# Kernel tuning notes

Measured on AMD Instinct MI355X. Metric: run time of the kernel, lower is better.

Reference implementation:

```python
import jax, jax.numpy as jnp
import numpy as np

VTH = 1.0  # config['v_threshold']
DT = 1.0


def spike_fn(x):
    # forward of ActFun_adp: heaviside(mem - vth)
    return (x > 0).astype(x.dtype)


def setup_inputs() -> dict:
    key = jax.random.key(0)
    k0, k1, k2, k3, k4 = jax.random.split(key, 5)
    B, T, D, H, O = 256, 250, 700, 1024, 20
    input_data = jax.random.normal(k0, (B, T, D), dtype=jnp.float32)
    # dense_1: nn.Linear(700, hidden) default init ~ U(-1/sqrt(D), 1/sqrt(D)); normal/sqrt(D) is an equivalent-scale stand-in
    W1 = jax.random.normal(k1, (H, D), dtype=jnp.float32) / np.sqrt(D).astype(np.float32)
    b1 = jnp.zeros((H,), dtype=jnp.float32)
    tau_m1 = jax.random.uniform(k2, (H,), dtype=jnp.float32, minval=0.0, maxval=4.0)
    # dense_2: xavier_normal_ weight, zero bias
    W2 = jax.random.normal(k3, (O, H), dtype=jnp.float32) * np.sqrt(2.0 / (H + O)).astype(np.float32)
    b2 = jnp.zeros((O,), dtype=jnp.float32)
    tau_m2 = jax.random.uniform(k4, (O,), dtype=jnp.float32, minval=0.0, maxval=4.0)
    return {"input_data": input_data, "W1": W1, "b1": b1, "tau_m1": tau_m1,
            "W2": W2, "b2": b2, "tau_m2": tau_m2}


def reference(input_data, W1, b1, tau_m1, W2, b2, tau_m2):
    B, T, D = input_data.shape
    H = W1.shape[0]
    O = W2.shape[0]
    alpha1 = jax.nn.sigmoid(tau_m1)  # [H]
    alpha2 = jax.nn.sigmoid(tau_m2)  # [O]
    # dense_1 is time-invariant: precompute projections for all timesteps [T,B,H]
    d1_all = (jnp.einsum('btd,hd->bth', input_data, W1) + b1).transpose(1, 0, 2)

    def step(carry, xs):
        mem1, spk1, mem2, acc = carry
        d1_t, i = xs
        # LIF layer 1: soft reset via -vth*spike (mem_update_pra, R_m=1, dt=1)
        mem1 = mem1 * alpha1 + (1.0 - alpha1) * d1_t - VTH * spk1 * DT
        spk1 = spike_fn(mem1 - VTH)
        # readout integrator
        d2 = spk1 @ W2.T + b2
        mem2 = mem2 * alpha2 + (1.0 - alpha2) * d2
        # accumulate softmax for i > 10
        gate = jnp.where(i > 10, jnp.float32(1.0), jnp.float32(0.0))
        acc = acc + gate * jax.nn.softmax(mem2, axis=1)
        return (mem1, spk1, mem2, acc), None

    init = (jnp.zeros((B, H), jnp.float32), jnp.zeros((B, H), jnp.float32),
            jnp.zeros((B, O), jnp.float32), jnp.zeros((B, O), jnp.float32))
    (_, _, _, acc), _ = jax.lax.scan(step, init, (d1_all, jnp.arange(T)))
    return acc
```

## Files before the change

kernel.cpp:

```cpp
#include <hip/hip_runtime.h>
#include <hip/hip_bf16.h>

#define B_  256
#define T_  250
#define D_  700
#define H_  1024
#define O_  20
#define KP  704
#define M_  64000

typedef __attribute__((ext_vector_type(8))) short bf16x8;
typedef __attribute__((ext_vector_type(4))) float f32x4;

__device__ __forceinline__ void gl_lds16(const void* g, void* l) {
    __builtin_amdgcn_global_load_lds(
        (const __attribute__((address_space(1))) unsigned int*)g,
        (__attribute__((address_space(3))) unsigned int*)l, 16, 0, 0);
}

__global__ void split_convert(const float* __restrict__ src,
                              unsigned short* __restrict__ hi,
                              unsigned short* __restrict__ lo,
                              int M, int Kin, int Kout)
{
    int idx = blockIdx.x * blockDim.x + threadIdx.x;
    int chunks = Kout >> 3;
    int total = M * chunks;
    if (idx >= total) return;
    int m  = idx / chunks;
    int c  = idx - m * chunks;
    int d0 = c << 3;
    float x[8];
    if (d0 + 8 <= Kin) {
        const float4* p = (const float4*)(src + (long)m * Kin + d0);
        float4 v0 = p[0], v1 = p[1];
        x[0] = v0.x; x[1] = v0.y; x[2] = v0.z; x[3] = v0.w;
        x[4] = v1.x; x[5] = v1.y; x[6] = v1.z; x[7] = v1.w;
    } else {
#pragma unroll
        for (int e = 0; e < 8; ++e) {
            int d = d0 + e;
            x[e] = (d < Kin) ? src[(long)m * Kin + d] : 0.0f;
        }
    }
    unsigned short h8[8], l8[8];
#pragma unroll
    for (int e = 0; e < 8; ++e) {
        __hip_bfloat16 h = __float2bfloat16(x[e]);
        float hf = __bfloat162float(h);
        __hip_bfloat16 lv = __float2bfloat16(x[e] - hf);
        h8[e] = *(unsigned short*)&h;
        l8[e] = *(unsigned short*)&lv;
    }
    long ob = (long)m * Kout + d0;
    *(uint4*)(hi + ob) = *(uint4*)h8;
    *(uint4*)(lo + ob) = *(uint4*)l8;
}

__global__ __launch_bounds__(256, 4) void gemm_split(
    const unsigned short* __restrict__ Ahi, const unsigned short* __restrict__ Alo,
    const unsigned short* __restrict__ Bhi, const unsigned short* __restrict__ Blo,
    const float* __restrict__ bias, float* __restrict__ C)
{
    __shared__ __align__(16) unsigned short sAh[128 * 32];
    __shared__ __align__(16) unsigned short sAl[128 * 32];
    __shared__ __align__(16) unsigned short sBh[128 * 32];
    __shared__ __align__(16) unsigned short sBl[128 * 32];

    const int t    = threadIdx.x;
    const int nblk = blockIdx.x;
    const int mblk = blockIdx.y;
    const int wave = t >> 6, lane = t & 63;
    const int wr = wave >> 1, wc = wave & 1;

    f32x4 acc[4][4];
#pragma unroll
    for (int i = 0; i < 4; ++i)
#pragma unroll
        for (int j = 0; j < 4; ++j) acc[i][j] = (f32x4){0.f, 0.f, 0.f, 0.f};

    const long arow = (long)(mblk * 128 + (t >> 2)) * KP + (t & 3) * 8;
    const long brow = (long)(nblk * 128 + (t >> 2)) * KP + (t & 3) * 8;
    const int  l8   = t * 8;

    const int fr = lane & 15;
    const int fk = (lane >> 4) * 8;

    for (int ks = 0; ks < KP; ks += 32) {
        __syncthreads();
        gl_lds16(Ahi + arow + ks, &sAh[l8]);
        gl_lds16(Ahi + arow + 64 * KP + ks, &sAh[2048 + l8]);
        gl_lds16(Alo + arow + ks, &sAl[l8]);
        gl_lds16(Alo + arow + 64 * KP + ks, &sAl[2048 + l8]);
        gl_lds16(Bhi + brow + ks, &sBh[l8]);
        gl_lds16(Bhi + brow + 64 * KP + ks, &sBh[2048 + l8]);
        gl_lds16(Blo + brow + ks, &sBl[l8]);
        gl_lds16(Blo + brow + 64 * KP + ks, &sBl[2048 + l8]);
        __syncthreads();

        bf16x8 bh[4], bl[4];
#pragma unroll
        for (int j = 0; j < 4; ++j) {
            bh[j] = *(const bf16x8*)&sBh[(wc * 64 + j * 16 + fr) * 32 + fk];
            bl[j] = *(const bf16x8*)&sBl[(wc * 64 + j * 16 + fr) * 32 + fk];
        }
#pragma unroll
        for (int i = 0; i < 4; ++i) {
            bf16x8 ah = *(const bf16x8*)&sAh[(wr * 64 + i * 16 + fr) * 32 + fk];
            bf16x8 al = *(const bf16x8*)&sAl[(wr * 64 + i * 16 + fr) * 32 + fk];
#pragma unroll
            for (int j = 0; j < 4; ++j)
                acc[i][j] = __builtin_amdgcn_mfma_f32_16x16x32_bf16(ah, bh[j], acc[i][j], 0, 0, 0);
#pragma unroll
            for (int j = 0; j < 4; ++j)
                acc[i][j] = __builtin_amdgcn_mfma_f32_16x16x32_bf16(ah, bl[j], acc[i][j], 0, 0, 0);
#pragma unroll
            for (int j = 0; j < 4; ++j)
                acc[i][j] = __builtin_amdgcn_mfma_f32_16x16x32_bf16(al, bh[j], acc[i][j], 0, 0, 0);
        }
    }

    const int r0 = mblk * 128 + wr * 64 + (lane >> 4) * 4;
    const int c0 = nblk * 128 + wc * 64 + (lane & 15);
#pragma unroll
    for (int j = 0; j < 4; ++j) {
        int col = c0 + j * 16;
        float bv = bias[col];
#pragma unroll
        for (int i = 0; i < 4; ++i) {
            int row = r0 + i * 16;
#pragma unroll
            for (int r = 0; r < 4; ++r)
                C[(long)(row + r) * H_ + col] = acc[i][j][r] + bv;
        }
    }
}

__global__ __launch_bounds__(256) void lif_spikes(
    const float* __restrict__ d1,
    const float* __restrict__ tau1,
    unsigned long long* __restrict__ spk)
{
    const int b    = blockIdx.y;
    const int h    = blockIdx.x * 256 + threadIdx.x;
    const int lane = threadIdx.x & 63;
    const int widx = blockIdx.x * 4 + (threadIdx.x >> 6);

    float tv  = tau1[h];
    float a1  = 1.0f / (1.0f + __expf(-tv));
    float om1 = 1.0f - a1;
    float mem = 0.f, sp = 0.f;

    const float* dp = d1 + (long)b * T_ * H_ + h;
    unsigned long long* op = spk + (long)b * T_ * 16 + widx;

    float p0 = dp[0],        p1 = dp[1L * H_], p2 = dp[2L * H_];
    float p3 = dp[3L * H_],  p4 = dp[4L * H_], p5 = dp[5L * H_];

    for (int ts = 0; ts < T_; ++ts) {
        float cur = p0;
        p0 = p1; p1 = p2; p2 = p3; p3 = p4; p4 = p5;
        int nts = ts + 6; nts = (nts < T_) ? nts : (T_ - 1);
        p5 = dp[(long)nts * H_];

        mem = mem * a1 + om1 * cur - sp;
        sp  = (mem > 1.0f) ? 1.0f : 0.0f;
        unsigned long long msk = __ballot(mem > 1.0f);
        if (lane == 0) op[(long)ts * 16] = msk;
    }
}

__global__ __launch_bounds__(256) void readout_dots(
    const unsigned long long* __restrict__ spk,
    const float* __restrict__ W2,
    float* __restrict__ d2t)
{
    const int t = threadIdx.x, wave = t >> 6, lane = t & 63;

    float w2r[5][16];
#pragma unroll
    for (int oo = 0; oo < 5; ++oo)
#pragma unroll
        for (int q = 0; q < 4; ++q)
            *(float4*)&w2r[oo][4 * q] =
                *(const float4*)&W2[(wave * 5 + oo) * H_ + lane * 16 + 4 * q];

    const int rbase = blockIdx.x * 32;
    int b0 = rbase / T_;
    int ts0 = rbase - b0 * T_;

    for (int i = 0; i < 32; i += 2) {
        int r0 = rbase + i, r1 = r0 + 1;
        unsigned long long bw0 = spk[(long)r0 * 16 + (lane >> 2)];
        unsigned long long bw1 = spk[(long)r1 * 16 + (lane >> 2)];
        unsigned int bits0 = (unsigned int)(bw0 >> ((lane & 3) * 16)) & 0xFFFFu;
        unsigned int bits1 = (unsigned int)(bw1 >> ((lane & 3) * 16)) & 0xFFFFu;
        float pa0[5] = {0, 0, 0, 0, 0}, pa1[5] = {0, 0, 0, 0, 0};
#pragma unroll
        for (int j = 0; j < 16; ++j) {
            float f0 = (bits0 >> j) & 1u ? 1.0f : 0.0f;
            float f1 = (bits1 >> j) & 1u ? 1.0f : 0.0f;
#pragma unroll
            for (int oo = 0; oo < 5; ++oo) {
                pa0[oo] = fmaf(f0, w2r[oo][j], pa0[oo]);
                pa1[oo] = fmaf(f1, w2r[oo][j], pa1[oo]);
            }
        }
#pragma unroll
        for (int m = 1; m < 64; m <<= 1)
#pragma unroll
            for (int oo = 0; oo < 5; ++oo) {
                pa0[oo] += __shfl_xor(pa0[oo], m, 64);
                pa1[oo] += __shfl_xor(pa1[oo], m, 64);
            }
        if (lane == 0) {
            int bA = b0, tsA = ts0 + i;
            if (tsA >= T_) { tsA -= T_; bA += 1; }
            int bB = bA, tsB = tsA + 1;
            if (tsB >= T_) { tsB = 0; bB += 1; }
#pragma unroll
            for (int oo = 0; oo < 5; ++oo) {
                d2t[(long)(wave * 5 + oo) * M_ + tsA * 256 + bA] = pa0[oo];
                d2t[(long)(wave * 5 + oo) * M_ + tsB * 256 + bB] = pa1[oo];
            }
        }
    }
}

__global__ __launch_bounds__(64) void mem2_scan(
    const float* __restrict__ d2t,
    const float* __restrict__ tau2, const float* __restrict__ b2,
    float* __restrict__ m2t)
{
    const int o = blockIdx.x;
    const int b = blockIdx.y * 64 + threadIdx.x;
    float tv  = tau2[o];
    float a2  = 1.0f / (1.0f + __expf(-tv));
    float om2 = 1.0f - a2;
    float bv  = b2[o];

    const float* dp = d2t + (long)o * M_ + b;
    float*       mp = m2t + (long)o * M_ + b;
    float mem = 0.f;

    float p0 = dp[0], p1 = dp[256], p2 = dp[512], p3 = dp[768];
    for (int ts = 0; ts < T_; ++ts) {
        float cur = p0; p0 = p1; p1 = p2; p2 = p3;
        int nts = ts + 4; nts = (nts < T_) ? nts : (T_ - 1);
        p3 = dp[(long)nts * 256];
        mem = mem * a2 + om2 * (cur + bv);
        mp[(long)ts * 256] = mem;
    }
}

__global__ __launch_bounds__(256) void softmax_acc(
    const float* __restrict__ m2t,
    float* __restrict__ out)
{
    __shared__ float sp[T_][O_];
    const int b  = blockIdx.x;
    const int ts = threadIdx.x;

    if (ts < T_) {
        if (ts > 10) {
            float m[O_];
#pragma unroll
            for (int o = 0; o < O_; ++o)
                m[o] = m2t[(long)o * M_ + ts * 256 + b];
            float mx = m[0];
#pragma unroll
            for (int o = 1; o < O_; ++o) mx = fmaxf(mx, m[o]);
            float s = 0.f;
#pragma unroll
            for (int o = 0; o < O_; ++o) { m[o] = __expf(m[o] - mx); s += m[o]; }
            float inv = 1.0f / s;
#pragma unroll
            for (int o = 0; o < O_; ++o) sp[ts][o] = m[o] * inv;
        } else {
#pragma unroll
            for (int o = 0; o < O_; ++o) sp[ts][o] = 0.f;
        }
    }
    __syncthreads();
    if (ts < O_) {
        float s = 0.f;
        for (int k = 11; k < T_; ++k) s += sp[k][ts];
        out[b * O_ + ts] = s;
    }
}

extern "C" void kernel_launch(void* const* d_in, const int* in_sizes, int n_in,
                              void* d_out, int out_size, void* d_ws, size_t ws_size,
                              hipStream_t stream)
{
    const float* X    = (const float*)d_in[0];
    const float* W1   = (const float*)d_in[1];
    const float* b1   = (const float*)d_in[2];
    const float* tau1 = (const float*)d_in[3];
    const float* W2   = (const float*)d_in[4];
    const float* b2   = (const float*)d_in[5];
    const float* tau2 = (const float*)d_in[6];
    float* out = (float*)d_out;

    unsigned short* Xhi  = (unsigned short*)d_ws;
    unsigned short* Xlo  = Xhi + (long)M_ * KP;
    unsigned short* W1hi = Xlo + (long)M_ * KP;
    unsigned short* W1lo = W1hi + (long)H_ * KP;
    float* d1 = (float*)(W1lo + (long)H_ * KP);

    unsigned long long* spk = (unsigned long long*)Xhi;
    float* d2t = (float*)Xlo;
    float* m2t = d2t + (long)O_ * M_;

    {
        int chunks = M_ * (KP / 8);
        split_convert<<<(chunks + 255) / 256, 256, 0, stream>>>(X, Xhi, Xlo, M_, D_, KP);
    }
    {
        int chunks = H_ * (KP / 8);
        split_convert<<<(chunks + 255) / 256, 256, 0, stream>>>(W1, W1hi, W1lo, H_, D_, KP);
    }

    {
        dim3 grid(H_ / 128, M_ / 128);
        gemm_split<<<grid, 256, 0, stream>>>(Xhi, Xlo, W1hi, W1lo, b1, d1);
    }

    {
        dim3 grid(H_ / 256, B_);
        lif_spikes<<<grid, 256, 0, stream>>>(d1, tau1, spk);
    }

    readout_dots<<<M_ / 32, 256, 0, stream>>>(spk, W2, d2t);

    {
        dim3 grid(O_, 4);
        mem2_scan<<<grid, 64, 0, stream>>>(d2t, tau2, b2, m2t);
    }

    softmax_acc<<<B_, 256, 0, stream>>>(m2t, out);
}
```

Before: 795.7 us.

## Replace split-bf16 GEMM with 256x256 double-buffered, swizzled, XCD-remapped kernel

Swaps the 128x128 split-bf16 GEMM for a 256x256 tile kernel with 512 threads, double-buffered LDS, and prefetch of the next K slice while the current one runs on MFMA. The LDS layout is XOR-swizzled to avoid bank conflicts, block IDs are remapped across the 8 XCDs for L2 locality, and s_setprio raises priority during MFMA bursts. The aim is more operand reuse per tile and overlap of global loads with compute. The cost is much higher register and LDS pressure (128 KB LDS, 32 accumulators per thread), and the hand-placed waitcnt and barrier scheduling is fragile.

```diff
diff --git a/kernel.cpp b/kernel.cpp
--- a/kernel.cpp
+++ b/kernel.cpp
@@ -8,6 +8,7 @@
 #define O_  20
 #define KP  704
 #define M_  64000
+#define NT  22
 
 typedef __attribute__((ext_vector_type(8))) short bf16x8;
 typedef __attribute__((ext_vector_type(4))) float f32x4;
@@ -57,77 +58,120 @@
     *(uint4*)(lo + ob) = *(uint4*)l8;
 }
 
-__global__ __launch_bounds__(256, 4) void gemm_split(
+#define MF(a,b,c) (c) = __builtin_amdgcn_mfma_f32_16x16x32_bf16((a),(b),(c),0,0,0)
+
+__global__ __launch_bounds__(512, 2) void gemm256(
     const unsigned short* __restrict__ Ahi, const unsigned short* __restrict__ Alo,
     const unsigned short* __restrict__ Bhi, const unsigned short* __restrict__ Blo,
     const float* __restrict__ bias, float* __restrict__ C)
 {
-    __shared__ __align__(16) unsigned short sAh[128 * 32];
-    __shared__ __align__(16) unsigned short sAl[128 * 32];
-    __shared__ __align__(16) unsigned short sBh[128 * 32];
-    __shared__ __align__(16) unsigned short sBl[128 * 32];
+    __shared__ __align__(16) unsigned short sAh[2 * 8192];
+    __shared__ __align__(16) unsigned short sAl[2 * 8192];
+    __shared__ __align__(16) unsigned short sBh[2 * 8192];
+    __shared__ __align__(16) unsigned short sBl[2 * 8192];
+
+    const int bid = blockIdx.x;
+    const int wg  = (bid & 7) * 125 + (bid >> 3);
+    const int mblk = wg >> 2;
+    const int nblk = wg & 3;
 
     const int t    = threadIdx.x;
-    const int nblk = blockIdx.x;
-    const int mblk = blockIdx.y;
     const int wave = t >> 6, lane = t & 63;
-    const int wr = wave >> 1, wc = wave & 1;
-
-    f32x4 acc[4][4];
-#pragma unroll
-    for (int i = 0; i < 4; ++i)
+    const int wr = wave >> 2, wc = wave & 3;
+
+    const int  ch0    = wave * 2;
+    const int  rowoff = lane >> 2;
+    const int  slotl  = (lane & 3) ^ ((lane >> 3) & 3);
+    const long GCH    = 16L * KP;
+    const long gArow  = (long)(mblk * 256 + rowoff) * KP + slotl * 8;
+    const long gBrow  = (long)(nblk * 256 + rowoff) * KP + slotl * 8;
+    const int  ldsl   = ch0 * 512 + lane * 8;
+
+    const int fr   = lane & 15, fq = lane >> 4;
+    const int fxor = ((fq ^ ((fr >> 1) & 3)) << 3);
+    const int abase = (wr * 128 + fr) * 32 + fxor;
+    const int bbase = (wc * 64 + fr) * 32 + fxor;
+
+    f32x4 acc[8][4];
+#pragma unroll
+    for (int i = 0; i < 8; ++i)
 #pragma unroll
         for (int j = 0; j < 4; ++j) acc[i][j] = (f32x4){0.f, 0.f, 0.f, 0.f};
 
-    const long arow = (long)(mblk * 128 + (t >> 2)) * KP + (t & 3) * 8;
-    const long brow = (long)(nblk * 128 + (t >> 2)) * KP + (t & 3) * 8;
-    const int  l8   = t * 8;
-
-    const int fr = lane & 15;
-    const int fk = (lane >> 4) * 8;
-
-    for (int ks = 0; ks < KP; ks += 32) {
-        __syncthreads();
-        gl_lds16(Ahi + arow + ks, &sAh[l8]);
-        gl_lds16(Ahi + arow + 64 * KP + ks, &sAh[2048 + l8]);
-        gl_lds16(Alo + arow + ks, &sAl[l8]);
-        gl_lds16(Alo + arow + 64 * KP + ks, &sAl[2048 + l8]);
-        gl_lds16(Bhi + brow + ks, &sBh[l8]);
-        gl_lds16(Bhi + brow + 64 * KP + ks, &sBh[2048 + l8]);
-        gl_lds16(Blo + brow + ks, &sBl[l8]);
-        gl_lds16(Blo + brow + 64 * KP + ks, &sBl[2048 + l8]);
-        __syncthreads();
+    gl_lds16(Ahi + gArow + ch0 * GCH,       &sAh[ldsl]);
+    gl_lds16(Ahi + gArow + (ch0 + 1) * GCH, &sAh[ldsl + 512]);
+    gl_lds16(Bhi + gBrow + ch0 * GCH,       &sBh[ldsl]);
+    gl_lds16(Bhi + gBrow + (ch0 + 1) * GCH, &sBh[ldsl + 512]);
+    gl_lds16(Alo + gArow + ch0 * GCH,       &sAl[ldsl]);
+    gl_lds16(Alo + gArow + (ch0 + 1) * GCH, &sAl[ldsl + 512]);
+    gl_lds16(Blo + gBrow + ch0 * GCH,       &sBl[ldsl]);
+    gl_lds16(Blo + gBrow + (ch0 + 1) * GCH, &sBl[ldsl + 512]);
+    asm volatile("s_waitcnt vmcnt(0)" ::: "memory");
+    __builtin_amdgcn_s_barrier();
+
+    for (int tt = 0; tt < NT; ++tt) {
+        const int  cur = (tt & 1) ? 8192 : 0;
+        const int  nxt = 8192 - cur;
+        const long ksn = (long)(tt + 1) * 32;
+        const bool pf  = (tt + 1 < NT);
 
         bf16x8 bh[4], bl[4];
 #pragma unroll
-        for (int j = 0; j < 4; ++j) {
-            bh[j] = *(const bf16x8*)&sBh[(wc * 64 + j * 16 + fr) * 32 + fk];
-            bl[j] = *(const bf16x8*)&sBl[(wc * 64 + j * 16 + fr) * 32 + fk];
-        }
-#pragma unroll
-        for (int i = 0; i < 4; ++i) {
-            bf16x8 ah = *(const bf16x8*)&sAh[(wr * 64 + i * 16 + fr) * 32 + fk];
-            bf16x8 al = *(const bf16x8*)&sAl[(wr * 64 + i * 16 + fr) * 32 + fk];
-#pragma unroll
-            for (int j = 0; j < 4; ++j)
-                acc[i][j] = __builtin_amdgcn_mfma_f32_16x16x32_bf16(ah, bh[j], acc[i][j], 0, 0, 0);
-#pragma unroll
-            for (int j = 0; j < 4; ++j)
-                acc[i][j] = __builtin_amdgcn_mfma_f32_16x16x32_bf16(ah, bl[j], acc[i][j], 0, 0, 0);
-#pragma unroll
-            for (int j = 0; j < 4; ++j)
-                acc[i][j] = __builtin_amdgcn_mfma_f32_16x16x32_bf16(al, bh[j], acc[i][j], 0, 0, 0);
-        }
-    }
-
-    const int r0 = mblk * 128 + wr * 64 + (lane >> 4) * 4;
-    const int c0 = nblk * 128 + wc * 64 + (lane & 15);
+        for (int p = 0; p < 4; ++p) {
+            const int i0 = 2 * p, i1 = 2 * p + 1;
+            bf16x8 ah0 = *(const bf16x8*)&sAh[cur + abase + i0 * 512];
+            bf16x8 ah1 = *(const bf16x8*)&sAh[cur + abase + i1 * 512];
+            bf16x8 al0 = *(const bf16x8*)&sAl[cur + abase + i0 * 512];
+            bf16x8 al1 = *(const bf16x8*)&sAl[cur + abase + i1 * 512];
+            if (p == 0) {
+#pragma unroll
+                for (int j = 0; j < 4; ++j) {
+                    bh[j] = *(const bf16x8*)&sBh[cur + bbase + j * 512];
+                    bl[j] = *(const bf16x8*)&sBl[cur + bbase + j * 512];
+                }
+            }
+            if (p == 0 && pf) {
+                gl_lds16(Ahi + gArow + ch0 * GCH + ksn,       &sAh[nxt + ldsl]);
+                gl_lds16(Ahi + gArow + (ch0 + 1) * GCH + ksn, &sAh[nxt + ldsl + 512]);
+                gl_lds16(Bhi + gBrow + ch0 * GCH + ksn,       &sBh[nxt + ldsl]);
+                gl_lds16(Bhi + gBrow + (ch0 + 1) * GCH + ksn, &sBh[nxt + ldsl + 512]);
+            }
+            if (p == 1 && pf) {
+                gl_lds16(Alo + gArow + ch0 * GCH + ksn,       &sAl[nxt + ldsl]);
+                gl_lds16(Alo + gArow + (ch0 + 1) * GCH + ksn, &sAl[nxt + ldsl + 512]);
+                gl_lds16(Blo + gBrow + ch0 * GCH + ksn,       &sBl[nxt + ldsl]);
+                gl_lds16(Blo + gBrow + (ch0 + 1) * GCH + ksn, &sBl[nxt + ldsl + 512]);
+            }
+            __builtin_amdgcn_s_barrier();
+            asm volatile("s_waitcnt lgkmcnt(0)" ::: "memory");
+            __builtin_amdgcn_sched_barrier(0);
+            __builtin_amdgcn_s_setprio(1);
+#pragma unroll
+            for (int j = 0; j < 4; ++j) MF(ah0, bh[j], acc[i0][j]);
+#pragma unroll
+            for (int j = 0; j < 4; ++j) MF(ah1, bh[j], acc[i1][j]);
+#pragma unroll
+            for (int j = 0; j < 4; ++j) MF(ah0, bl[j], acc[i0][j]);
+#pragma unroll
+            for (int j = 0; j < 4; ++j) MF(ah1, bl[j], acc[i1][j]);
+#pragma unroll
+            for (int j = 0; j < 4; ++j) MF(al0, bh[j], acc[i0][j]);
+#pragma unroll
+            for (int j = 0; j < 4; ++j) MF(al1, bh[j], acc[i1][j]);
+            __builtin_amdgcn_s_setprio(0);
+            if (p == 3) asm volatile("s_waitcnt vmcnt(0)" ::: "memory");
+            __builtin_amdgcn_s_barrier();
+        }
+    }
+
+    const int r0 = mblk * 256 + wr * 128 + fq * 4;
+    const int cc = nblk * 256 + wc * 64 + fr;
 #pragma unroll
     for (int j = 0; j < 4; ++j) {
-        int col = c0 + j * 16;
+        int col = cc + j * 16;
         float bv = bias[col];
 #pragma unroll
-        for (int i = 0; i < 4; ++i) {
+        for (int i = 0; i < 8; ++i) {
             int row = r0 + i * 16;
 #pragma unroll
             for (int r = 0; r < 4; ++r)
@@ -321,10 +365,7 @@
         split_convert<<<(chunks + 255) / 256, 256, 0, stream>>>(W1, W1hi, W1lo, H_, D_, KP);
     }
 
-    {
-        dim3 grid(H_ / 128, M_ / 128);
-        gemm_split<<<grid, 256, 0, stream>>>(Xhi, Xlo, W1hi, W1lo, b1, d1);
-    }
+    gemm256<<<dim3(1000), dim3(512), 0, stream>>>(Xhi, Xlo, W1hi, W1lo, b1, d1);
 
     {
         dim3 grid(H_ / 256, B_);
```

Result: no change. 795.6 us (-0.0%).
